# Performance work log

Hardware: AMD Instinct MI355X
Metric: run time of the kernel (lower is better)

Reference implementation:

```python
import jax, jax.numpy as jnp
import numpy as np

B, T, L, D, H = 8, 4, 512, 512, 8
HD = D // H
THR = 1.0
BETA = 0.5
EPS = 1e-5


def heaviside(x):
    return (x >= 0).astype(x.dtype)


def bn_eval(x, g, b, rm, rv):
    # BatchNorm1d in eval mode applied on the last dim
    return (x - rm) * (g * jax.lax.rsqrt(rv + EPS)) + b


def lif(x_btld):
    # snntorch Leaky(beta=0.5, threshold=1, reset='subtract'), mem init 0, scan over T
    xs = jnp.moveaxis(x_btld, 1, 0)  # (T,B,L,D)

    def step(mem, xt):
        reset = heaviside(mem - THR)          # reset from previous mem (detached in torch)
        mem = BETA * mem + xt - reset * THR
        spk = heaviside(mem - THR)
        return mem, spk

    _, spks = jax.lax.scan(step, jnp.zeros_like(xs[0]), xs)
    return jnp.moveaxis(spks, 0, 1)


def setup_inputs() -> dict:
    key = jax.random.key(0)
    ks = jax.random.split(key, 24)
    s = D ** -0.5
    inp = {
        "x": jax.random.normal(ks[0], (B, T, L, D), jnp.float32),
        "q_w": jax.random.normal(ks[1], (D, D), jnp.float32) * s,
        "q_g": jax.random.normal(ks[2], (D,), jnp.float32),
        "q_b": jax.random.normal(ks[3], (D,), jnp.float32),
        "q_rm": jax.random.normal(ks[4], (D,), jnp.float32),
        "q_rv": jax.random.uniform(ks[5], (D,), jnp.float32),
        "k_w": jax.random.normal(ks[6], (D, D), jnp.float32) * s,
        "k_g": jax.random.normal(ks[7], (D,), jnp.float32),
        "k_b": jax.random.normal(ks[8], (D,), jnp.float32),
        "k_rm": jax.random.normal(ks[9], (D,), jnp.float32),
        "k_rv": jax.random.uniform(ks[10], (D,), jnp.float32),
        "v_w": jax.random.normal(ks[11], (D, D), jnp.float32) * s,
        "v_g": jax.random.normal(ks[12], (D,), jnp.float32),
        "v_b": jax.random.normal(ks[13], (D,), jnp.float32),
        "v_rm": jax.random.normal(ks[14], (D,), jnp.float32),
        "v_rv": jax.random.uniform(ks[15], (D,), jnp.float32),
        "o_w": jax.random.normal(ks[16], (D, D), jnp.float32) * s,
        "o_bias": jax.random.normal(ks[17], (D,), jnp.float32),
        "o_g": jax.random.normal(ks[18], (D,), jnp.float32),
        "o_b": jax.random.normal(ks[19], (D,), jnp.float32),
        "o_rm": jax.random.normal(ks[20], (D,), jnp.float32),
        "o_rv": jax.random.uniform(ks[21], (D,), jnp.float32),
    }
    return inp


def reference(x, q_w, q_g, q_b, q_rm, q_rv, k_w, k_g, k_b, k_rm, k_rv,
              v_w, v_g, v_b, v_rm, v_rv, o_w, o_bias, o_g, o_b, o_rm, o_rv):
    scale = HD ** -0.5
    # Q path: linear -> BN -> LIF (binary {0,1})
    q = bn_eval(jnp.einsum('btld,ed->btle', x, q_w), q_g, q_b, q_rm, q_rv)
    q = lif(q)
    # K path: linear -> BN -> ReLU (continuous)
    k = jax.nn.relu(bn_eval(jnp.einsum('btld,ed->btle', x, k_w), k_g, k_b, k_rm, k_rv))
    # V path: linear -> BN -> ternary {-1,0,+1}
    v = bn_eval(jnp.einsum('btld,ed->btle', x, v_w), v_g, v_b, v_rm, v_rv)
    v = heaviside(v - THR) - heaviside(-v - THR)
    # split heads: (B,T,H,L,hd)
    sh = lambda a: a.reshape(B, T, L, H, HD).transpose(0, 1, 3, 2, 4)
    q, k, v = sh(q), sh(k), sh(v)
    attn = jnp.einsum('bthld,bthmd->bthlm', q, k) * scale
    out = jnp.einsum('bthlm,bthmd->bthld', attn, v)
    out = out.transpose(0, 1, 3, 2, 4).reshape(B, T, L, D)
    out = jnp.einsum('btld,ed->btle', out, o_w) + o_bias
    out = bn_eval(out, o_g, o_b, o_rm, o_rv)
    return lif(out)
```

## Files before the change

kernel.cpp:

```cpp
#include <hip/hip_runtime.h>
#include <math.h>
#include <stdint.h>

#define Bb 8
#define Tt 4
#define Ll 512
#define Dd 512
#define Hh 8
#define HDd 64
#define Mm (Bb*Tt*Ll)

typedef _Float16 f16;
typedef _Float16 f16x8 __attribute__((ext_vector_type(8)));
typedef _Float16 f16x4 __attribute__((ext_vector_type(4)));
typedef float f32x16 __attribute__((ext_vector_type(16)));

#define LO_SCALE 2048.0f
#define LO_INV   4.8828125e-4f

__device__ __forceinline__ void gload16(const void* g, void* l) {
  __builtin_amdgcn_global_load_lds(
      (const __attribute__((address_space(1))) unsigned int*)(uintptr_t)g,
      (__attribute__((address_space(3))) unsigned int*)(uintptr_t)l,
      16, 0, 0);
}

struct SplitArgs {
  const float* src[5];
  f16* hi[5];
  f16* lo[5];
};

__global__ void split_k(SplitArgs s) {
  int i = blockIdx.x * 256 + threadIdx.x;
  int seg, base;
  if (i < 1048576) { seg = 0; base = i; }
  else { int r = i - 1048576; seg = 1 + (r >> 15); base = r & 32767; }
  const float* sp = s.src[seg] + (size_t)base * 8;
  float4 v0 = *(const float4*)sp;
  float4 v1 = *(const float4*)(sp + 4);
  float a[8] = {v0.x, v0.y, v0.z, v0.w, v1.x, v1.y, v1.z, v1.w};
  f16x8 hv, lv;
  #pragma unroll
  for (int e = 0; e < 8; ++e) {
    f16 hh = (f16)a[e];
    hv[e] = hh;
    lv[e] = (f16)((a[e] - (float)hh) * LO_SCALE);
  }
  *(f16x8*)(s.hi[seg] + (size_t)base * 8) = hv;
  *(f16x8*)(s.lo[seg] + (size_t)base * 8) = lv;
}

struct GArgs {
  const f16 *Ah, *Al;
  const f16 *Wh0, *Wl0, *Wh1, *Wl1, *Wh2, *Wl2;
  const float *g0,*b0,*rm0,*rv0;
  const float *g1,*b1,*rm1,*rv1;
  const float *g2,*b2,*rm2,*rv2;
  const float* bias;
  f16*   oq;
  float* ok;
  f16*   ov;
  float* oo;
};

#define SMEM_BYTES 65536

template<int MODE>
__global__ __launch_bounds__(256, 2)
void gemm_f16(GArgs ar) {
  extern __shared__ __align__(16) char smem[];
  float (*TS)[133] = (float(*)[133])smem;

  const int tid = threadIdx.x;
  const int lane = tid & 63, wid = tid >> 6;

  const int bid = blockIdx.x;
  int bx, by;
  if (MODE == 0) { const int sw = (bid & 7) * 192 + (bid >> 3); bx = sw % 12; by = sw / 12; }
  else           { const int sw = (bid & 7) * 64  + (bid >> 3); bx = sw & 3;  by = sw >> 2; }

  const int seg = (MODE == 0) ? (bx >> 2) : 0;
  const int lc0 = (MODE == 0) ? ((bx & 3) << 7) : (bx << 7);
  const int b = by >> 4, lc32 = by & 15;

  const f16* Wh = (seg == 0 ? ar.Wh0 : (seg == 1 ? ar.Wh1 : ar.Wh2));
  const f16* Wl = (seg == 0 ? ar.Wl0 : (seg == 1 ? ar.Wl1 : ar.Wl2));
  const float* gp  = (seg == 0 ? ar.g0  : (seg == 1 ? ar.g1  : ar.g2));
  const float* bp  = (seg == 0 ? ar.b0  : (seg == 1 ? ar.b1  : ar.b2));
  const float* rmp = (seg == 0 ? ar.rm0 : (seg == 1 ? ar.rm1 : ar.rm2));
  const float* rvp = (seg == 0 ? ar.rv0 : (seg == 1 ? ar.rv1 : ar.rv2));

  const int sr = lane >> 2, skc = lane & 3;
  const int skcs = skc ^ (sr & 3);
  const int frow = lane & 31, khalf = lane >> 5;
  const int wmr = wid >> 1, wnc = wid & 1;

  f32x16 acc_h[2][2], acc_l[2][2];
  #pragma unroll
  for (int i = 0; i < 2; ++i)
    #pragma unroll
    for (int j = 0; j < 2; ++j) {
      acc_h[i][j] = (f32x16)0.0f;
      acc_l[i][j] = (f32x16)0.0f;
    }

  #define STAGE(k0_, slot_)                                                        \
    {                                                                              \
      char* sb = smem + (slot_) * 32768;                                           \
      _Pragma("unroll")                                                            \
      for (int i = 0; i < 2; ++i) {                                                \
        const int r = i * 64 + wid * 16 + sr;                                      \
        const int growA = (((b << 2) + (r >> 5)) << 9) + (lc32 << 5) + (r & 31);   \
        const size_t goA = (size_t)growA * Dd + (k0_) + skcs * 8;                  \
        const size_t goB = (size_t)(lc0 + r) * Dd + (k0_) + skcs * 8;              \
        const int lb = i * 2048 + wid * 512;                                       \
        gload16(ar.Ah + goA, (f16*)sb + lb);                                       \
        gload16(ar.Al + goA, (f16*)(sb + 8192) + lb);                              \
        gload16(Wh + goB, (f16*)(sb + 16384) + lb);                                \
        gload16(Wl + goB, (f16*)(sb + 24576) + lb);                                \
      }                                                                            \
    }

  STAGE(0, 0);
  __syncthreads();

  for (int t = 0; t < 16; ++t) {
    const int cur = t & 1;
    const f16* Ahs = (const f16*)(smem + cur * 32768);
    const f16* Als = Ahs + 4096;
    const f16* Bhs = Ahs + 8192;
    const f16* Bls = Ahs + 12288;

    if (t < 15) STAGE((t + 1) * 32, cur ^ 1);

    f16x8 ah[2][2], al[2][2], bh[2][2], bl[2][2];
    #pragma unroll
    for (int mi = 0; mi < 2; ++mi) {
      const int r = wmr * 64 + mi * 32 + frow;
      #pragma unroll
      for (int ks = 0; ks < 2; ++ks) {
        const int cin = (khalf + 2 * ks) ^ (lane & 3);
        const int ad = r * 32 + cin * 8;
        ah[mi][ks] = *(const f16x8*)&Ahs[ad];
        al[mi][ks] = *(const f16x8*)&Als[ad];
      }
    }
    #pragma unroll
    for (int nj = 0; nj < 2; ++nj) {
      const int r = wnc * 64 + nj * 32 + frow;
      #pragma unroll
      for (int ks = 0; ks < 2; ++ks) {
        const int cin = (khalf + 2 * ks) ^ (lane & 3);
        const int ad = r * 32 + cin * 8;
        bh[nj][ks] = *(const f16x8*)&Bhs[ad];
        bl[nj][ks] = *(const f16x8*)&Bls[ad];
      }
    }
    #pragma unroll
    for (int ks = 0; ks < 2; ++ks)
      #pragma unroll
      for (int mi = 0; mi < 2; ++mi)
        #pragma unroll
        for (int nj = 0; nj < 2; ++nj) {
          acc_h[mi][nj] = __builtin_amdgcn_mfma_f32_32x32x16_f16(ah[mi][ks], bh[nj][ks], acc_h[mi][nj], 0, 0, 0);
          acc_l[mi][nj] = __builtin_amdgcn_mfma_f32_32x32x16_f16(ah[mi][ks], bl[nj][ks], acc_l[mi][nj], 0, 0, 0);
          acc_l[mi][nj] = __builtin_amdgcn_mfma_f32_32x32x16_f16(al[mi][ks], bh[nj][ks], acc_l[mi][nj], 0, 0, 0);
        }
    __syncthreads();
  }
  #undef STAGE

  float scl[2], shc[2];
  #pragma unroll
  for (int nj = 0; nj < 2; ++nj) {
    const int c = lc0 + wnc * 64 + nj * 32 + frow;
    double S = (double)gp[c] / sqrt((double)rvp[c] + 1e-5);
    double Sh = (double)bp[c] - (double)rmp[c] * S;
    if (MODE == 1) Sh += (double)ar.bias[c] * S;
    scl[nj] = (float)S; shc[nj] = (float)Sh;
  }

  if (MODE == 0 && seg != 0) {
    #pragma unroll
    for (int mi = 0; mi < 2; ++mi)
      #pragma unroll
      for (int nj = 0; nj < 2; ++nj)
        #pragma unroll
        for (int r = 0; r < 16; ++r) {
          const int row32 = (r & 3) + 8 * (r >> 2) + 4 * khalf;
          const int tr = wmr * 64 + mi * 32 + row32;
          const int grow = (((b << 2) + (tr >> 5)) << 9) + (lc32 << 5) + (tr & 31);
          const int col = lc0 + wnc * 64 + nj * 32 + frow;
          float val = acc_h[mi][nj][r] + acc_l[mi][nj][r] * LO_INV;
          float y = val * scl[nj] + shc[nj];
          if (seg == 1) ar.ok[(size_t)grow * Dd + col] = fmaxf(y, 0.f);
          else ar.ov[(size_t)grow * Dd + col] =
                   (f16)((y >= 1.f ? 1.f : 0.f) - (-y >= 1.f ? 1.f : 0.f));
        }
    return;
  }

  #pragma unroll
  for (int half = 0; half < 2; ++half) {
    if (wnc == half) {
      #pragma unroll
      for (int mi = 0; mi < 2; ++mi)
        #pragma unroll
        for (int nj = 0; nj < 2; ++nj)
          #pragma unroll
          for (int q = 0; q < 4; ++q) {
            float4 yv;
            float* yp = &yv.x;
            #pragma unroll
            for (int rr = 0; rr < 4; ++rr) {
              const int r = q * 4 + rr;
              float val = acc_h[mi][nj][r] + acc_l[mi][nj][r] * LO_INV;
              yp[rr] = val * scl[nj] + shc[nj];
            }
            *(float4*)&TS[nj * 32 + frow][wmr * 64 + mi * 32 + 8 * q + 4 * khalf] = yv;
          }
    }
    __syncthreads();
    const int cc4 = (tid & 15) << 2;
    #pragma unroll
    for (int rr = 0; rr < 2; ++rr) {
      const int rl = (tid >> 4) + (rr << 4);
      float mm[4] = {0.f, 0.f, 0.f, 0.f};
      #pragma unroll
      for (int t = 0; t < 4; ++t) {
        const int trow = t * 32 + rl;
        float sp[4];
        #pragma unroll
        for (int c = 0; c < 4; ++c) {
          float y = TS[cc4 + c][trow];
          float rst = (mm[c] >= 1.f) ? 1.f : 0.f;
          mm[c] = 0.5f * mm[c] + y - rst;
          sp[c] = (mm[c] >= 1.f) ? 1.f : 0.f;
        }
        const size_t go = ((size_t)((((b << 2) + t) << 9) + (lc32 << 5) + rl)) * Dd
                          + lc0 + (half << 6) + cc4;
        if (MODE == 0) {
          f16x4 s4;
          s4[0] = (f16)sp[0]; s4[1] = (f16)sp[1]; s4[2] = (f16)sp[2]; s4[3] = (f16)sp[3];
          *(f16x4*)(ar.oq + go) = s4;
        } else {
          *(float4*)(ar.oo + go) = make_float4(sp[0], sp[1], sp[2], sp[3]);
        }
      }
    }
    __syncthreads();
  }
}

__global__ __launch_bounds__(256)
void attn_g(const float* __restrict__ ks, const f16* __restrict__ vs,
            float* __restrict__ pG) {
  const int bt = blockIdx.x, h = blockIdx.y, c = blockIdx.z;
  const float* kp = ks + (size_t)bt * Ll * Dd + h * HDd;
  const f16* vp = vs + (size_t)bt * Ll * Dd + h * HDd;

  __shared__ float KS[64][68];
  __shared__ float VS[64][68];
  const int tid = threadIdx.x;
  const int te = tid & 15, td = tid >> 4;

  float gacc[4][4];
  #pragma unroll
  for (int i = 0; i < 4; ++i)
    #pragma unroll
    for (int j = 0; j < 4; ++j) gacc[i][j] = 0.f;

  for (int mt = 0; mt < 2; ++mt) {
    const int m0 = c * 128 + mt * 64;
    #pragma unroll
    for (int it = 0; it < 4; ++it) {
      int fidx = it * 256 + tid;
      int row = fidx >> 4, fq = fidx & 15;
      *(float4*)&KS[row][fq << 2] = *(const float4*)(kp + (size_t)(m0 + row) * Dd + (fq << 2));
    }
    #pragma unroll
    for (int it = 0; it < 2; ++it) {
      int fidx = it * 256 + tid;
      int row = fidx >> 3, c8 = fidx & 7;
      f16x8 hv = *(const f16x8*)(vp + (size_t)(m0 + row) * Dd + (c8 << 3));
      *(float4*)&VS[row][c8 << 3] = make_float4(hv[0], hv[1], hv[2], hv[3]);
      *(float4*)&VS[row][(c8 << 3) + 4] = make_float4(hv[4], hv[5], hv[6], hv[7]);
    }
    __syncthreads();
    #pragma unroll 4
    for (int mm = 0; mm < 64; ++mm) {
      float4 k4 = *(const float4*)&KS[mm][te << 2];
      float4 v4 = *(const float4*)&VS[mm][td << 2];
      const float kk[4] = {k4.x, k4.y, k4.z, k4.w};
      const float vv[4] = {v4.x, v4.y, v4.z, v4.w};
      #pragma unroll
      for (int i = 0; i < 4; ++i)
        #pragma unroll
        for (int j = 0; j < 4; ++j)
          gacc[i][j] = fmaf(kk[i], vv[j], gacc[i][j]);
    }
    __syncthreads();
  }
  float* out = pG + (((size_t)(bt * 8 + h) * 4 + c) << 12);
  #pragma unroll
  for (int i = 0; i < 4; ++i)
    *(float4*)&out[((te << 2) + i) * 64 + (td << 2)] =
        make_float4(gacc[i][0] * 0.125f, gacc[i][1] * 0.125f,
                    gacc[i][2] * 0.125f, gacc[i][3] * 0.125f);
}

__global__ __launch_bounds__(256)
void attn_o(const f16* __restrict__ qs, const float* __restrict__ pG,
            f16* __restrict__ ahi, f16* __restrict__ alo) {
  const int bt = blockIdx.x, h = blockIdx.y, lc = blockIdx.z;
  __shared__ float G[64][68];
  __shared__ float QS[64][68];
  const int tid = threadIdx.x;

  const float* pg = pG + (((size_t)(bt * 8 + h) * 4) << 12);
  #pragma unroll
  for (int rep = 0; rep < 4; ++rep) {
    int t4 = rep * 256 + tid;
    int e = t4 >> 4, dq = t4 & 15;
    int off = e * 64 + (dq << 2);
    float4 s0 = *(const float4*)(pg + off);
    float4 s1 = *(const float4*)(pg + 4096 + off);
    float4 s2 = *(const float4*)(pg + 8192 + off);
    float4 s3 = *(const float4*)(pg + 12288 + off);
    *(float4*)&G[e][dq << 2] = make_float4(s0.x + s1.x + s2.x + s3.x,
                                           s0.y + s1.y + s2.y + s3.y,
                                           s0.z + s1.z + s2.z + s3.z,
                                           s0.w + s1.w + s2.w + s3.w);
  }
  __syncthreads();

  const f16* qp = qs + (size_t)bt * Ll * Dd + h * HDd;
  const int lr = tid >> 2, dg = tid & 3;

  for (int l0 = 0; l0 < 128; l0 += 64) {
    #pragma unroll
    for (int it = 0; it < 2; ++it) {
      int fidx = it * 256 + tid;
      int row = fidx >> 3, c8 = fidx & 7;
      f16x8 hv = *(const f16x8*)(qp + (size_t)(lc * 128 + l0 + row) * Dd + (c8 << 3));
      *(float4*)&QS[row][c8 << 3] = make_float4(hv[0], hv[1], hv[2], hv[3]);
      *(float4*)&QS[row][(c8 << 3) + 4] = make_float4(hv[4], hv[5], hv[6], hv[7]);
    }
    __syncthreads();
    float oacc[16];
    #pragma unroll
    for (int j = 0; j < 16; ++j) oacc[j] = 0.f;
    for (int ee = 0; ee < 64; ++ee) {
      float qv = QS[lr][ee];
      #pragma unroll
      for (int jq = 0; jq < 4; ++jq) {
        float4 g4 = *(const float4*)&G[ee][(dg << 4) + (jq << 2)];
        oacc[jq * 4 + 0] = fmaf(qv, g4.x, oacc[jq * 4 + 0]);
        oacc[jq * 4 + 1] = fmaf(qv, g4.y, oacc[jq * 4 + 1]);
        oacc[jq * 4 + 2] = fmaf(qv, g4.z, oacc[jq * 4 + 2]);
        oacc[jq * 4 + 3] = fmaf(qv, g4.w, oacc[jq * 4 + 3]);
      }
    }
    f16x8 h0, l0v, h1, l1v;
    #pragma unroll
    for (int t = 0; t < 8; ++t) {
      float v = oacc[t];
      f16 hh = (f16)v;
      h0[t] = hh; l0v[t] = (f16)((v - (float)hh) * LO_SCALE);
      float v2 = oacc[8 + t];
      f16 hh2 = (f16)v2;
      h1[t] = hh2; l1v[t] = (f16)((v2 - (float)hh2) * LO_SCALE);
    }
    size_t ob = ((size_t)bt * Ll + lc * 128 + l0 + lr) * Dd + h * HDd + (dg << 4);
    *(f16x8*)(ahi + ob) = h0;
    *(f16x8*)(ahi + ob + 8) = h1;
    *(f16x8*)(alo + ob) = l0v;
    *(f16x8*)(alo + ob + 8) = l1v;
    __syncthreads();
  }
}

extern "C" void kernel_launch(void* const* d_in, const int* in_sizes, int n_in,
                              void* d_out, int out_size, void* d_ws, size_t ws_size,
                              hipStream_t stream) {
  const float* x    = (const float*)d_in[0];
  const float* q_w  = (const float*)d_in[1];
  const float* q_g  = (const float*)d_in[2];
  const float* q_b  = (const float*)d_in[3];
  const float* q_rm = (const float*)d_in[4];
  const float* q_rv = (const float*)d_in[5];
  const float* k_w  = (const float*)d_in[6];
  const float* k_g  = (const float*)d_in[7];
  const float* k_b  = (const float*)d_in[8];
  const float* k_rm = (const float*)d_in[9];
  const float* k_rv = (const float*)d_in[10];
  const float* v_w  = (const float*)d_in[11];
  const float* v_g  = (const float*)d_in[12];
  const float* v_b  = (const float*)d_in[13];
  const float* v_rm = (const float*)d_in[14];
  const float* v_rv = (const float*)d_in[15];
  const float* o_w  = (const float*)d_in[16];
  const float* o_bias = (const float*)d_in[17];
  const float* o_g  = (const float*)d_in[18];
  const float* o_b  = (const float*)d_in[19];
  const float* o_rm = (const float*)d_in[20];
  const float* o_rv = (const float*)d_in[21];

  char* wsb = (char*)d_ws;
  const size_t R16 = 16777216;
  f16*   xhi  = (f16*)wsb;
  f16*   xlo  = (f16*)(wsb + R16);
  f16*   qspk = (f16*)(wsb + 2 * R16);
  float* kbuf = (float*)(wsb + 3 * R16);
  f16*   vbuf = (f16*)(wsb + 5 * R16);
  float* pG   = (float*)(wsb + 6 * R16);
  f16*   wsp  = (f16*)(wsb + 7 * R16);
  f16* qwh = wsp;            f16* qwl = wsp + 262144;
  f16* kwh = wsp + 2*262144; f16* kwl = wsp + 3*262144;
  f16* vwh = wsp + 4*262144; f16* vwl = wsp + 5*262144;
  f16* owh = wsp + 6*262144; f16* owl = wsp + 7*262144;
  f16* ahi = xhi;
  f16* alo = xlo;

  SplitArgs sa;
  sa.src[0] = x;   sa.hi[0] = xhi; sa.lo[0] = xlo;
  sa.src[1] = q_w; sa.hi[1] = qwh; sa.lo[1] = qwl;
  sa.src[2] = k_w; sa.hi[2] = kwh; sa.lo[2] = kwl;
  sa.src[3] = v_w; sa.hi[3] = vwh; sa.lo[3] = vwl;
  sa.src[4] = o_w; sa.hi[4] = owh; sa.lo[4] = owl;
  split_k<<<4608, 256, 0, stream>>>(sa);

  GArgs a1;
  a1.Ah = xhi; a1.Al = xlo;
  a1.Wh0 = qwh; a1.Wl0 = qwl; a1.Wh1 = kwh; a1.Wl1 = kwl; a1.Wh2 = vwh; a1.Wl2 = vwl;
  a1.g0 = q_g; a1.b0 = q_b; a1.rm0 = q_rm; a1.rv0 = q_rv;
  a1.g1 = k_g; a1.b1 = k_b; a1.rm1 = k_rm; a1.rv1 = k_rv;
  a1.g2 = v_g; a1.b2 = v_b; a1.rm2 = v_rm; a1.rv2 = v_rv;
  a1.bias = nullptr;
  a1.oq = qspk; a1.ok = kbuf; a1.ov = vbuf; a1.oo = nullptr;
  gemm_f16<0><<<1536, 256, SMEM_BYTES, stream>>>(a1);

  attn_g<<<dim3(32, 8, 4), 256, 0, stream>>>(kbuf, vbuf, pG);
  attn_o<<<dim3(32, 8, 4), 256, 0, stream>>>(qspk, pG, ahi, alo);

  GArgs a2;
  a2.Ah = ahi; a2.Al = alo;
  a2.Wh0 = owh; a2.Wl0 = owl; a2.Wh1 = owh; a2.Wl1 = owl; a2.Wh2 = owh; a2.Wl2 = owl;
  a2.g0 = o_g; a2.b0 = o_b; a2.rm0 = o_rm; a2.rv0 = o_rv;
  a2.g1 = o_g; a2.b1 = o_b; a2.rm1 = o_rm; a2.rv1 = o_rv;
  a2.g2 = o_g; a2.b2 = o_b; a2.rm2 = o_rm; a2.rv2 = o_rv;
  a2.bias = o_bias;
  a2.oq = nullptr; a2.ok = nullptr; a2.ov = nullptr; a2.oo = (float*)d_out;
  gemm_f16<1><<<512, 256, SMEM_BYTES, stream>>>(a2);
}
```

Measured before the change: 307.2 us.

## Drop double-buffered LDS staging for single buffer and change swizzle

Replaces the two-slot LDS ping-pong pipeline in the split-f16 GEMM with a single 32 KB buffer that is loaded and synchronized each k-step. Shared memory shrinks to about 34 KB, which may allow more resident blocks per CU. The XOR swizzle pattern for LDS writes and reads is also changed to depend on row pairs, aiming to reduce bank conflicts. In exchange, global-to-LDS loads no longer overlap with MFMA compute within a block, and each k-step now needs two barriers.

```diff
diff --git a/kernel.cpp b/kernel.cpp
--- a/kernel.cpp
+++ b/kernel.cpp
@@ -64,12 +64,16 @@
   float* oo;
 };
 
-#define SMEM_BYTES 65536
+#define SMEM_BYTES 34048
 
 template<int MODE>
 __global__ __launch_bounds__(256, 2)
 void gemm_f16(GArgs ar) {
   extern __shared__ __align__(16) char smem[];
+  f16* Ah_s = (f16*)smem;
+  f16* Al_s = (f16*)(smem + 8192);
+  f16* Bh_s = (f16*)(smem + 16384);
+  f16* Bl_s = (f16*)(smem + 24576);
   float (*TS)[133] = (float(*)[133])smem;
 
   const int tid = threadIdx.x;
@@ -92,8 +96,9 @@
   const float* rvp = (seg == 0 ? ar.rv0 : (seg == 1 ? ar.rv1 : ar.rv2));
 
   const int sr = lane >> 2, skc = lane & 3;
-  const int skcs = skc ^ (sr & 3);
+  const int skcs = skc ^ ((sr >> 1) & 3);
   const int frow = lane & 31, khalf = lane >> 5;
+  const int rsw = (frow >> 1) & 3;
   const int wmr = wid >> 1, wnc = wid & 1;
 
   f32x16 acc_h[2][2], acc_l[2][2];
@@ -105,34 +110,21 @@
       acc_l[i][j] = (f32x16)0.0f;
     }
 
-  #define STAGE(k0_, slot_)                                                        \
-    {                                                                              \
-      char* sb = smem + (slot_) * 32768;                                           \
-      _Pragma("unroll")                                                            \
-      for (int i = 0; i < 2; ++i) {                                                \
-        const int r = i * 64 + wid * 16 + sr;                                      \
-        const int growA = (((b << 2) + (r >> 5)) << 9) + (lc32 << 5) + (r & 31);   \
-        const size_t goA = (size_t)growA * Dd + (k0_) + skcs * 8;                  \
-        const size_t goB = (size_t)(lc0 + r) * Dd + (k0_) + skcs * 8;              \
-        const int lb = i * 2048 + wid * 512;                                       \
-        gload16(ar.Ah + goA, (f16*)sb + lb);                                       \
-        gload16(ar.Al + goA, (f16*)(sb + 8192) + lb);                              \
-        gload16(Wh + goB, (f16*)(sb + 16384) + lb);                                \
-        gload16(Wl + goB, (f16*)(sb + 24576) + lb);                                \
-      }                                                                            \
-    }
-
-  STAGE(0, 0);
-  __syncthreads();
-
-  for (int t = 0; t < 16; ++t) {
-    const int cur = t & 1;
-    const f16* Ahs = (const f16*)(smem + cur * 32768);
-    const f16* Als = Ahs + 4096;
-    const f16* Bhs = Ahs + 8192;
-    const f16* Bls = Ahs + 12288;
-
-    if (t < 15) STAGE((t + 1) * 32, cur ^ 1);
+  for (int k0 = 0; k0 < Dd; k0 += 32) {
+    __syncthreads();
+    #pragma unroll
+    for (int i = 0; i < 2; ++i) {
+      const int r = i * 64 + wid * 16 + sr;
+      const int growA = (((b << 2) + (r >> 5)) << 9) + (lc32 << 5) + (r & 31);
+      const size_t goA = (size_t)growA * Dd + k0 + skcs * 8;
+      const size_t goB = (size_t)(lc0 + r) * Dd + k0 + skcs * 8;
+      const int lb = i * 2048 + wid * 512;
+      gload16(ar.Ah + goA, Ah_s + lb);
+      gload16(ar.Al + goA, Al_s + lb);
+      gload16(Wh + goB, Bh_s + lb);
+      gload16(Wl + goB, Bl_s + lb);
+    }
+    __syncthreads();
 
     f16x8 ah[2][2], al[2][2], bh[2][2], bl[2][2];
     #pragma unroll
@@ -140,10 +132,10 @@
       const int r = wmr * 64 + mi * 32 + frow;
       #pragma unroll
       for (int ks = 0; ks < 2; ++ks) {
-        const int cin = (khalf + 2 * ks) ^ (lane & 3);
+        const int cin = (khalf + 2 * ks) ^ rsw;
         const int ad = r * 32 + cin * 8;
-        ah[mi][ks] = *(const f16x8*)&Ahs[ad];
-        al[mi][ks] = *(const f16x8*)&Als[ad];
+        ah[mi][ks] = *(const f16x8*)&Ah_s[ad];
+        al[mi][ks] = *(const f16x8*)&Al_s[ad];
       }
     }
     #pragma unroll
@@ -151,10 +143,10 @@
       const int r = wnc * 64 + nj * 32 + frow;
       #pragma unroll
       for (int ks = 0; ks < 2; ++ks) {
-        const int cin = (khalf + 2 * ks) ^ (lane & 3);
+        const int cin = (khalf + 2 * ks) ^ rsw;
         const int ad = r * 32 + cin * 8;
-        bh[nj][ks] = *(const f16x8*)&Bhs[ad];
-        bl[nj][ks] = *(const f16x8*)&Bls[ad];
+        bh[nj][ks] = *(const f16x8*)&Bh_s[ad];
+        bl[nj][ks] = *(const f16x8*)&Bl_s[ad];
       }
     }
     #pragma unroll
@@ -167,9 +159,7 @@
           acc_l[mi][nj] = __builtin_amdgcn_mfma_f32_32x32x16_f16(ah[mi][ks], bl[nj][ks], acc_l[mi][nj], 0, 0, 0);
           acc_l[mi][nj] = __builtin_amdgcn_mfma_f32_32x32x16_f16(al[mi][ks], bh[nj][ks], acc_l[mi][nj], 0, 0, 0);
         }
-    __syncthreads();
-  }
-  #undef STAGE
+  }
 
   float scl[2], shc[2];
   #pragma unroll
@@ -201,6 +191,7 @@
     return;
   }
 
+  __syncthreads();
   #pragma unroll
   for (int half = 0; half < 2; ++half) {
     if (wnc == half) {
```

New measurement: 297.0 us. 3.3% less time.
